# Performance work log

Measured on AMD Instinct MI355X. Metric: run time of the kernel, lower is better.

Reference implementation:

```python
import jax, jax.numpy as jnp
import numpy as np

N_HEAD = 16
N_KV_GROUP = 4
WINDOW = 256


def setup_inputs() -> dict:
    key = jax.random.key(0)
    ks = jax.random.split(key, 5)
    B, T, C = 2, 2048, 1024
    KV = C // N_HEAD * N_KV_GROUP  # 256
    s = 0.02
    return {
        "x": jax.random.normal(ks[0], (B, T, C), jnp.float32),
        "Wq": jax.random.normal(ks[1], (C, C), jnp.float32) * s,
        "bq": jnp.zeros((C,), jnp.float32),
        "Wk": jax.random.normal(ks[2], (C, KV), jnp.float32) * s,
        "bk": jnp.zeros((KV,), jnp.float32),
        "Wv": jax.random.normal(ks[3], (C, KV), jnp.float32) * s,
        "bv": jnp.zeros((KV,), jnp.float32),
        "Wo": jax.random.normal(ks[4], (C, C), jnp.float32) * s,
        "bo": jnp.zeros((C,), jnp.float32),
    }


def reference(x, Wq, bq, Wk, bk, Wv, bv, Wo, bo):
    B, T, C = x.shape
    hd = C // N_HEAD  # head dim = 64
    n_rep = N_HEAD // N_KV_GROUP

    q = x @ Wq + bq                      # [B,T,C]
    k = x @ Wk + bk                      # [B,T,KV]
    v = x @ Wv + bv

    q = q.reshape(B, T, N_HEAD, hd).transpose(0, 2, 1, 3)       # [B,H,T,d]
    k = k.reshape(B, T, N_KV_GROUP, hd).transpose(0, 2, 1, 3)   # [B,G,T,d]
    v = v.reshape(B, T, N_KV_GROUP, hd).transpose(0, 2, 1, 3)

    # GQA: repeat_interleave kv heads along head dim
    k_rep = jnp.repeat(k, n_rep, axis=1)                         # [B,H,T,d]
    v_rep = jnp.repeat(v, n_rep, axis=1)

    att = jnp.einsum("bhqd,bhkd->bhqk", q, k_rep) / jnp.sqrt(jnp.float32(hd))

    # causal + sliding window band mask: q position i attends to j in [i-WINDOW, i]
    i = jnp.arange(T)[:, None]
    j = jnp.arange(T)[None, :]
    band = (j <= i) & (j >= i - WINDOW)                           # [T,T]
    att = jnp.where(band[None, None], att, jnp.float32(-jnp.inf))

    att = jax.nn.softmax(att, axis=-1)
    y = jnp.einsum("bhqk,bhkd->bhqd", att, v_rep)                 # [B,H,T,d]
    y = y.transpose(0, 2, 1, 3).reshape(B, T, C)
    return y @ Wo + bo
```

## Files before the change

kernel.cpp:

```cpp
#include <hip/hip_runtime.h>
#include <hip/hip_bf16.h>

#define TT 2048
#define CC 1024
#define KVD 256
#define QKVD 1536

typedef __bf16 bf16x8 __attribute__((ext_vector_type(8)));
typedef float f32x4 __attribute__((ext_vector_type(4)));

__device__ __forceinline__ void gload_lds16(const __hip_bfloat16* g, __hip_bfloat16* l) {
  __builtin_amdgcn_global_load_lds(
      (const __attribute__((address_space(1))) unsigned int*)g,
      (__attribute__((address_space(3))) unsigned int*)l, 16, 0, 0);
}


__global__ __launch_bounds__(256) void k_prep(const float* __restrict__ x,
                                              const float* __restrict__ Wq,
                                              const float* __restrict__ Wk,
                                              const float* __restrict__ Wv,
                                              const float* __restrict__ Wo,
                                              const float* __restrict__ bq,
                                              const float* __restrict__ bk,
                                              const float* __restrict__ bv,
                                              __hip_bfloat16* __restrict__ xbf,
                                              __hip_bfloat16* __restrict__ wqkvT,
                                              __hip_bfloat16* __restrict__ woT,
                                              float* __restrict__ bqkv) {
  const int bxid = blockIdx.x;
  if (bxid < 4096) {
    size_t idx = ((size_t)bxid * 256 + threadIdx.x) * 4;
    float4 v = *(const float4*)(x + idx);
    xbf[idx + 0] = __float2bfloat16(v.x);
    xbf[idx + 1] = __float2bfloat16(v.y);
    xbf[idx + 2] = __float2bfloat16(v.z);
    xbf[idx + 3] = __float2bfloat16(v.w);
    return;
  }
  if (bxid == 4736) {
    for (int i = threadIdx.x; i < 1536; i += 256) {
      float v;
      if (i < 1024)      v = bq[i];
      else if (i < 1280) v = bk[i - 1024];
      else               v = bv[i - 1280];
      bqkv[i] = v;
    }
    return;
  }
  __shared__ float tile[64][65];
  const float* src;
  int ncols, k0, n0;
  __hip_bfloat16* dst;
  if (bxid < 4480) {
    const int idx = bxid - 4096;
    k0 = (idx & 15) * 64;
    n0 = (idx >> 4) * 64;
    dst = wqkvT;
    if (n0 < 1024)      { src = Wq; ncols = 1024; }
    else if (n0 < 1280) { src = Wk - 1024; ncols = 256; }
    else                { src = Wv - 1280; ncols = 256; }
  } else {
    const int idx = bxid - 4480;
    k0 = (idx & 15) * 64;
    n0 = (idx >> 4) * 64;
    dst = woT; src = Wo; ncols = 1024;
  }
  const int rw = threadIdx.x >> 6;
  const int cl = threadIdx.x & 63;
#pragma unroll
  for (int i = 0; i < 16; ++i) {
    const int kr = rw + i * 4;
    tile[kr][cl] = src[(size_t)(k0 + kr) * ncols + n0 + cl];
  }
  __syncthreads();
#pragma unroll
  for (int i = 0; i < 16; ++i) {
    const int nr = rw + i * 4;
    dst[(size_t)(n0 + nr) * 1024 + k0 + cl] = __float2bfloat16(tile[cl][nr]);
  }
}


__global__ __launch_bounds__(256, 3) void k_gemm1(const __hip_bfloat16* __restrict__ A,
                                                  const __hip_bfloat16* __restrict__ BT,
                                                  const float* __restrict__ bias,
                                                  __hip_bfloat16* __restrict__ C,
                                                  __hip_bfloat16* __restrict__ vtg) {
  __shared__ __hip_bfloat16 As[128][64];
  __shared__ __hip_bfloat16 Bs[128][64];

  const int tid  = threadIdx.x;
  const int m0   = blockIdx.y * 128;
  const int n0   = blockIdx.x * 128;
  const int w    = tid >> 6;
  const int lane = tid & 63;
  const int quad = lane >> 4;
  const int l16  = lane & 15;
  const int wm   = (w >> 1) * 64;
  const int wn   = (w & 1) * 64;

  const int dl_r = lane >> 3;
  const int dl_c = (lane & 7) ^ dl_r;

  const __hip_bfloat16* gA = A + (size_t)(m0 + w * 32 + dl_r) * 1024 + dl_c * 8;
  const __hip_bfloat16* gB = BT + (size_t)(n0 + w * 32 + dl_r) * 1024 + dl_c * 8;

  f32x4 acc[4][4] = {};

  for (int kt = 0; kt < 16; ++kt) {
    const int k0 = kt << 6;
#pragma unroll
    for (int rr = 0; rr < 4; ++rr) {
      gload_lds16(gA + k0 + (size_t)(rr * 8) * 1024, &As[w * 32 + rr * 8][0]);
      gload_lds16(gB + k0 + (size_t)(rr * 8) * 1024, &Bs[w * 32 + rr * 8][0]);
    }
    __syncthreads();

#pragma unroll
    for (int ks = 0; ks < 2; ++ks) {
      const int cb = (ks << 2) + quad;
      bf16x8 fa[4], fb[4];
#pragma unroll
      for (int i = 0; i < 4; ++i)
        fa[i] = *(const bf16x8*)&As[wm + i * 16 + l16][(cb ^ (l16 & 7)) << 3];
#pragma unroll
      for (int j = 0; j < 4; ++j)
        fb[j] = *(const bf16x8*)&Bs[wn + j * 16 + l16][(cb ^ (l16 & 7)) << 3];
#pragma unroll
      for (int i = 0; i < 4; ++i)
#pragma unroll
        for (int j = 0; j < 4; ++j)
          acc[i][j] = __builtin_amdgcn_mfma_f32_16x16x32_bf16(fa[i], fb[j], acc[i][j], 0, 0, 0);
    }
    __syncthreads();
  }

#pragma unroll
  for (int j = 0; j < 4; ++j) {
    const int gn = n0 + wn + j * 16 + l16;
    const float bias_v = bias[gn];
    if (gn >= 1280) {
      const int dfull = gn - 1280;
      const int gg = dfull >> 6;
      const int dd = dfull & 63;
#pragma unroll
      for (int i = 0; i < 4; ++i) {
        const int gm = m0 + wm + i * 16 + quad * 4;
        const int bb = gm >> 11;
        const int tl = gm & 2047;
        __hip_bfloat16 tmp[4];
#pragma unroll
        for (int r = 0; r < 4; ++r) tmp[r] = __float2bfloat16(acc[i][j][r] + bias_v);
        *(uint2*)(vtg + ((size_t)((bb * 4 + gg) * 64 + dd)) * TT + tl) = *(const uint2*)tmp;
      }
    } else {
#pragma unroll
      for (int i = 0; i < 4; ++i) {
        const int gmb = m0 + wm + i * 16 + quad * 4;
#pragma unroll
        for (int r = 0; r < 4; ++r)
          C[(size_t)(gmb + r) * QKVD + gn] = __float2bfloat16(acc[i][j][r] + bias_v);
      }
    }
  }
}


__global__ __launch_bounds__(256, 4) void k_gemm2(const __hip_bfloat16* __restrict__ A,
                                                  const __hip_bfloat16* __restrict__ BT,
                                                  const float* __restrict__ bias,
                                                  float* __restrict__ C) {
  __shared__ __hip_bfloat16 As[64][64];
  __shared__ __hip_bfloat16 Bs[128][64];

  const int tid  = threadIdx.x;
  const int m0   = blockIdx.y * 64;
  const int n0   = blockIdx.x * 128;
  const int w    = tid >> 6;
  const int lane = tid & 63;
  const int quad = lane >> 4;
  const int l16  = lane & 15;
  const int wm   = (w >> 1) * 32;
  const int wn   = (w & 1) * 64;

  const int dl_r = lane >> 3;
  const int dl_c = (lane & 7) ^ dl_r;

  const __hip_bfloat16* gA = A + (size_t)(m0 + w * 16 + dl_r) * 1024 + dl_c * 8;
  const __hip_bfloat16* gB = BT + (size_t)(n0 + w * 32 + dl_r) * 1024 + dl_c * 8;

  f32x4 acc[2][4] = {};

  for (int kt = 0; kt < 16; ++kt) {
    const int k0 = kt << 6;
    gload_lds16(gA + k0,                     &As[w * 16][0]);
    gload_lds16(gA + k0 + (size_t)8 * 1024,  &As[w * 16 + 8][0]);
    gload_lds16(gB + k0,                     &Bs[w * 32][0]);
    gload_lds16(gB + k0 + (size_t)8 * 1024,  &Bs[w * 32 + 8][0]);
    gload_lds16(gB + k0 + (size_t)16 * 1024, &Bs[w * 32 + 16][0]);
    gload_lds16(gB + k0 + (size_t)24 * 1024, &Bs[w * 32 + 24][0]);
    __syncthreads();

#pragma unroll
    for (int ks = 0; ks < 2; ++ks) {
      const int cb = (ks << 2) + quad;
      bf16x8 fa[2], fb[4];
#pragma unroll
      for (int i = 0; i < 2; ++i)
        fa[i] = *(const bf16x8*)&As[wm + i * 16 + l16][(cb ^ (l16 & 7)) << 3];
#pragma unroll
      for (int j = 0; j < 4; ++j)
        fb[j] = *(const bf16x8*)&Bs[wn + j * 16 + l16][(cb ^ (l16 & 7)) << 3];
#pragma unroll
      for (int i = 0; i < 2; ++i)
#pragma unroll
        for (int j = 0; j < 4; ++j)
          acc[i][j] = __builtin_amdgcn_mfma_f32_16x16x32_bf16(fa[i], fb[j], acc[i][j], 0, 0, 0);
    }
    __syncthreads();
  }

#pragma unroll
  for (int j = 0; j < 4; ++j) {
    const int gn = n0 + wn + j * 16 + l16;
    const float bias_v = bias[gn];
#pragma unroll
    for (int i = 0; i < 2; ++i) {
      const int gmb = m0 + wm + i * 16 + quad * 4;
#pragma unroll
      for (int r = 0; r < 4; ++r)
        C[(size_t)(gmb + r) * CC + gn] = acc[i][j][r] + bias_v;
    }
  }
}


__global__ __launch_bounds__(256) void k_attn(const __hip_bfloat16* __restrict__ qkv,
                                              const __hip_bfloat16* __restrict__ vtg,
                                              __hip_bfloat16* __restrict__ y) {
  __shared__ __hip_bfloat16 Kb[2][64][64];
  __shared__ __hip_bfloat16 Vb[2][64][64];
  __shared__ __hip_bfloat16 Ps[4][16][72];

  const int t    = threadIdx.x;
  const int w    = t >> 6;
  const int lane = t & 63;
  const int quad = lane >> 4;
  const int l16  = lane & 15;
  const int bx   = blockIdx.x;
  const int h    = blockIdx.y;
  const int b    = blockIdx.z;
  const int g    = h >> 2;
  const int i0   = bx * 64;
  const int qrow      = i0 + w * 16 + l16;
  const int my_q_base = i0 + w * 16 + quad * 4;

  const int lrow = lane >> 3;
  const int cgl  = (lane & 7) ^ lrow;

  const __hip_bfloat16* kg =
      qkv + ((size_t)(b * TT + w * 16 + lrow)) * QKVD + 1024 + g * 64 + cgl * 8;
  const __hip_bfloat16* vg =
      vtg + ((size_t)((b * 4 + g) * 64 + w * 16 + lrow)) * TT + cgl * 8;

  bf16x8 fq[2];
  {
    const __hip_bfloat16* qp = qkv + ((size_t)(b * TT + qrow)) * QKVD + h * 64 + quad * 8;
    fq[0] = *(const bf16x8*)qp;
    fq[1] = *(const bf16x8*)(qp + 32);
  }

  float l_r[4] = {0.f, 0.f, 0.f, 0.f};
  f32x4 o_acc[4] = {};
  const float EC = 0.125f * 1.44269504f;

  const int c_lo = bx >= 4 ? bx - 4 : 0;

  {
    const size_t ko = (size_t)(c_lo * 64) * QKVD;
    gload_lds16(kg + ko,                    &Kb[0][w * 16][0]);
    gload_lds16(kg + ko + (size_t)8 * QKVD, &Kb[0][w * 16 + 8][0]);
    const int vo = c_lo * 64;
    gload_lds16(vg + vo,                  &Vb[0][w * 16][0]);
    gload_lds16(vg + vo + (size_t)8 * TT, &Vb[0][w * 16 + 8][0]);
  }

  int buf = 0;
  for (int c = c_lo; c <= bx; ++c) {
    __syncthreads();
    if (c < bx) {
      const size_t ko = (size_t)((c + 1) * 64) * QKVD;
      gload_lds16(kg + ko,                    &Kb[buf ^ 1][w * 16][0]);
      gload_lds16(kg + ko + (size_t)8 * QKVD, &Kb[buf ^ 1][w * 16 + 8][0]);
      const int vo = (c + 1) * 64;
      gload_lds16(vg + vo,                  &Vb[buf ^ 1][w * 16][0]);
      gload_lds16(vg + vo + (size_t)8 * TT, &Vb[buf ^ 1][w * 16 + 8][0]);
    }

    const int jc = c * 64;

    f32x4 sacc[4] = {};
#pragma unroll
    for (int ks = 0; ks < 2; ++ks) {
      const int sw = (((ks << 2) + quad) ^ (l16 & 7)) << 3;
#pragma unroll
      for (int nt = 0; nt < 4; ++nt) {
        const bf16x8 fk = *(const bf16x8*)&Kb[buf][nt * 16 + l16][sw];
        sacc[nt] = __builtin_amdgcn_mfma_f32_16x16x32_bf16(fq[ks], fk, sacc[nt], 0, 0, 0);
      }
    }

    if (c == bx) {
#pragma unroll
      for (int r = 0; r < 4; ++r) {
        const int gi = my_q_base + r;
#pragma unroll
        for (int nt = 0; nt < 4; ++nt) {
          const int key = jc + nt * 16 + l16;
          const float p = (key <= gi) ? exp2f(sacc[nt][r] * EC) : 0.f;
          l_r[r] += p;
          Ps[w][quad * 4 + r][nt * 16 + l16] = __float2bfloat16(p);
        }
      }
    } else if (bx >= 4 && c == c_lo) {
#pragma unroll
      for (int r = 0; r < 4; ++r) {
        const int glo = my_q_base + r - 256;
#pragma unroll
        for (int nt = 0; nt < 4; ++nt) {
          const int key = jc + nt * 16 + l16;
          const float p = (key >= glo) ? exp2f(sacc[nt][r] * EC) : 0.f;
          l_r[r] += p;
          Ps[w][quad * 4 + r][nt * 16 + l16] = __float2bfloat16(p);
        }
      }
    } else {
#pragma unroll
      for (int r = 0; r < 4; ++r)
#pragma unroll
        for (int nt = 0; nt < 4; ++nt) {
          const float p = exp2f(sacc[nt][r] * EC);
          l_r[r] += p;
          Ps[w][quad * 4 + r][nt * 16 + l16] = __float2bfloat16(p);
        }
    }

    const bf16x8 fp0 = *(const bf16x8*)&Ps[w][l16][quad * 8];
    const bf16x8 fp1 = *(const bf16x8*)&Ps[w][l16][32 + quad * 8];

#pragma unroll
    for (int ks = 0; ks < 2; ++ks) {
      const int sw = (((ks << 2) + quad) ^ (l16 & 7)) << 3;
#pragma unroll
      for (int jt = 0; jt < 4; ++jt) {
        const bf16x8 fv = *(const bf16x8*)&Vb[buf][jt * 16 + l16][sw];
        o_acc[jt] = __builtin_amdgcn_mfma_f32_16x16x32_bf16(ks == 0 ? fp0 : fp1, fv,
                                                            o_acc[jt], 0, 0, 0);
      }
    }
    buf ^= 1;
  }

#pragma unroll
  for (int r = 0; r < 4; ++r) {
#pragma unroll
    for (int d = 1; d < 16; d <<= 1) l_r[r] += __shfl_xor(l_r[r], d);
    const float inv = 1.f / l_r[r];
    __hip_bfloat16* yp = y + ((size_t)(b * TT + my_q_base + r)) * CC + h * 64 + l16;
#pragma unroll
    for (int jt = 0; jt < 4; ++jt)
      yp[jt * 16] = __float2bfloat16(o_acc[jt][r] * inv);
  }
}


extern "C" void kernel_launch(void* const* d_in, const int* in_sizes, int n_in,
                              void* d_out, int out_size, void* d_ws, size_t ws_size,
                              hipStream_t stream) {
  const float* x  = (const float*)d_in[0];
  const float* Wq = (const float*)d_in[1];
  const float* bq = (const float*)d_in[2];
  const float* Wk = (const float*)d_in[3];
  const float* bk = (const float*)d_in[4];
  const float* Wv = (const float*)d_in[5];
  const float* bv = (const float*)d_in[6];
  const float* Wo = (const float*)d_in[7];
  const float* bo = (const float*)d_in[8];
  float* out = (float*)d_out;

  char* ws = (char*)d_ws;
  const size_t M = 2 * TT;
  __hip_bfloat16* xbf   = (__hip_bfloat16*)(ws);
  __hip_bfloat16* qkv   = (__hip_bfloat16*)(ws + 8388608);
  __hip_bfloat16* ybf   = (__hip_bfloat16*)(ws + 20971520);
  __hip_bfloat16* wqkvT = (__hip_bfloat16*)(ws + 29360128);
  __hip_bfloat16* woT   = (__hip_bfloat16*)(ws + 32505856);
  float*          bqkv  = (float*)(ws + 34603008);
  __hip_bfloat16* vtg   = (__hip_bfloat16*)(ws + 34609152);

  k_prep<<<4737, 256, 0, stream>>>(x, Wq, Wk, Wv, Wo, bq, bk, bv,
                                   xbf, wqkvT, woT, bqkv);

  k_gemm1<<<dim3(QKVD / 128, M / 128), 256, 0, stream>>>(xbf, wqkvT, bqkv, qkv, vtg);

  k_attn<<<dim3(TT / 64, 16, 2), 256, 0, stream>>>(qkv, vtg, ybf);

  k_gemm2<<<dim3(CC / 128, M / 64), 256, 0, stream>>>(ybf, woT, bo, out);
}
```

Measured before the change: 145.5 us.

## Give each attention wave two query tiles and halve the block size

```diff
diff --git a/kernel.cpp b/kernel.cpp
--- a/kernel.cpp
+++ b/kernel.cpp
@@ -236,12 +236,12 @@
 }
 
 
-__global__ __launch_bounds__(256) void k_attn(const __hip_bfloat16* __restrict__ qkv,
+__global__ __launch_bounds__(128) void k_attn(const __hip_bfloat16* __restrict__ qkv,
                                               const __hip_bfloat16* __restrict__ vtg,
                                               __hip_bfloat16* __restrict__ y) {
   __shared__ __hip_bfloat16 Kb[2][64][64];
   __shared__ __hip_bfloat16 Vb[2][64][64];
-  __shared__ __hip_bfloat16 Ps[4][16][72];
+  __shared__ __hip_bfloat16 Ps[2][32][72];
 
   const int t    = threadIdx.x;
   const int w    = t >> 6;
@@ -253,37 +253,38 @@
   const int b    = blockIdx.z;
   const int g    = h >> 2;
   const int i0   = bx * 64;
-  const int qrow      = i0 + w * 16 + l16;
-  const int my_q_base = i0 + w * 16 + quad * 4;
 
   const int lrow = lane >> 3;
   const int cgl  = (lane & 7) ^ lrow;
 
   const __hip_bfloat16* kg =
-      qkv + ((size_t)(b * TT + w * 16 + lrow)) * QKVD + 1024 + g * 64 + cgl * 8;
+      qkv + ((size_t)(b * TT + w * 32 + lrow)) * QKVD + 1024 + g * 64 + cgl * 8;
   const __hip_bfloat16* vg =
-      vtg + ((size_t)((b * 4 + g) * 64 + w * 16 + lrow)) * TT + cgl * 8;
-
-  bf16x8 fq[2];
-  {
+      vtg + ((size_t)((b * 4 + g) * 64 + w * 32 + lrow)) * TT + cgl * 8;
+
+  bf16x8 fq[2][2];
+#pragma unroll
+  for (int it = 0; it < 2; ++it) {
+    const int qrow = i0 + w * 32 + it * 16 + l16;
     const __hip_bfloat16* qp = qkv + ((size_t)(b * TT + qrow)) * QKVD + h * 64 + quad * 8;
-    fq[0] = *(const bf16x8*)qp;
-    fq[1] = *(const bf16x8*)(qp + 32);
-  }
-
-  float l_r[4] = {0.f, 0.f, 0.f, 0.f};
-  f32x4 o_acc[4] = {};
+    fq[it][0] = *(const bf16x8*)qp;
+    fq[it][1] = *(const bf16x8*)(qp + 32);
+  }
+
+  float l_r[2][4] = {};
+  f32x4 o_acc[2][4] = {};
   const float EC = 0.125f * 1.44269504f;
 
   const int c_lo = bx >= 4 ? bx - 4 : 0;
 
   {
     const size_t ko = (size_t)(c_lo * 64) * QKVD;
-    gload_lds16(kg + ko,                    &Kb[0][w * 16][0]);
-    gload_lds16(kg + ko + (size_t)8 * QKVD, &Kb[0][w * 16 + 8][0]);
     const int vo = c_lo * 64;
-    gload_lds16(vg + vo,                  &Vb[0][w * 16][0]);
-    gload_lds16(vg + vo + (size_t)8 * TT, &Vb[0][w * 16 + 8][0]);
+#pragma unroll
+    for (int rr = 0; rr < 4; ++rr) {
+      gload_lds16(kg + ko + (size_t)(rr * 8) * QKVD, &Kb[0][w * 32 + rr * 8][0]);
+      gload_lds16(vg + vo + (size_t)(rr * 8) * TT,   &Vb[0][w * 32 + rr * 8][0]);
+    }
   }
 
   int buf = 0;
@@ -291,86 +292,106 @@
     __syncthreads();
     if (c < bx) {
       const size_t ko = (size_t)((c + 1) * 64) * QKVD;
-      gload_lds16(kg + ko,                    &Kb[buf ^ 1][w * 16][0]);
-      gload_lds16(kg + ko + (size_t)8 * QKVD, &Kb[buf ^ 1][w * 16 + 8][0]);
       const int vo = (c + 1) * 64;
-      gload_lds16(vg + vo,                  &Vb[buf ^ 1][w * 16][0]);
-      gload_lds16(vg + vo + (size_t)8 * TT, &Vb[buf ^ 1][w * 16 + 8][0]);
+#pragma unroll
+      for (int rr = 0; rr < 4; ++rr) {
+        gload_lds16(kg + ko + (size_t)(rr * 8) * QKVD, &Kb[buf ^ 1][w * 32 + rr * 8][0]);
+        gload_lds16(vg + vo + (size_t)(rr * 8) * TT,   &Vb[buf ^ 1][w * 32 + rr * 8][0]);
+      }
     }
 
     const int jc = c * 64;
 
-    f32x4 sacc[4] = {};
+    f32x4 sacc[2][4] = {};
+    __builtin_amdgcn_s_setprio(1);
 #pragma unroll
     for (int ks = 0; ks < 2; ++ks) {
       const int sw = (((ks << 2) + quad) ^ (l16 & 7)) << 3;
 #pragma unroll
       for (int nt = 0; nt < 4; ++nt) {
         const bf16x8 fk = *(const bf16x8*)&Kb[buf][nt * 16 + l16][sw];
-        sacc[nt] = __builtin_amdgcn_mfma_f32_16x16x32_bf16(fq[ks], fk, sacc[nt], 0, 0, 0);
-      }
-    }
-
-    if (c == bx) {
-#pragma unroll
-      for (int r = 0; r < 4; ++r) {
-        const int gi = my_q_base + r;
-#pragma unroll
-        for (int nt = 0; nt < 4; ++nt) {
-          const int key = jc + nt * 16 + l16;
-          const float p = (key <= gi) ? exp2f(sacc[nt][r] * EC) : 0.f;
-          l_r[r] += p;
-          Ps[w][quad * 4 + r][nt * 16 + l16] = __float2bfloat16(p);
+#pragma unroll
+        for (int it = 0; it < 2; ++it)
+          sacc[it][nt] = __builtin_amdgcn_mfma_f32_16x16x32_bf16(fq[it][ks], fk, sacc[it][nt], 0, 0, 0);
+      }
+    }
+    __builtin_amdgcn_s_setprio(0);
+
+#pragma unroll
+    for (int it = 0; it < 2; ++it) {
+      const int my_q_base = i0 + w * 32 + it * 16 + quad * 4;
+      if (c == bx) {
+#pragma unroll
+        for (int r = 0; r < 4; ++r) {
+          const int gi = my_q_base + r;
+#pragma unroll
+          for (int nt = 0; nt < 4; ++nt) {
+            const int key = jc + nt * 16 + l16;
+            const float p = (key <= gi) ? exp2f(sacc[it][nt][r] * EC) : 0.f;
+            l_r[it][r] += p;
+            Ps[w][it * 16 + quad * 4 + r][nt * 16 + l16] = __float2bfloat16(p);
+          }
         }
-      }
-    } else if (bx >= 4 && c == c_lo) {
-#pragma unroll
-      for (int r = 0; r < 4; ++r) {
-        const int glo = my_q_base + r - 256;
-#pragma unroll
-        for (int nt = 0; nt < 4; ++nt) {
-          const int key = jc + nt * 16 + l16;
-          const float p = (key >= glo) ? exp2f(sacc[nt][r] * EC) : 0.f;
-          l_r[r] += p;
-          Ps[w][quad * 4 + r][nt * 16 + l16] = __float2bfloat16(p);
+      } else if (bx >= 4 && c == c_lo) {
+#pragma unroll
+        for (int r = 0; r < 4; ++r) {
+          const int glo = my_q_base + r - 256;
+#pragma unroll
+          for (int nt = 0; nt < 4; ++nt) {
+            const int key = jc + nt * 16 + l16;
+            const float p = (key >= glo) ? exp2f(sacc[it][nt][r] * EC) : 0.f;
+            l_r[it][r] += p;
+            Ps[w][it * 16 + quad * 4 + r][nt * 16 + l16] = __float2bfloat16(p);
+          }
         }
-      }
-    } else {
-#pragma unroll
-      for (int r = 0; r < 4; ++r)
-#pragma unroll
-        for (int nt = 0; nt < 4; ++nt) {
-          const float p = exp2f(sacc[nt][r] * EC);
-          l_r[r] += p;
-          Ps[w][quad * 4 + r][nt * 16 + l16] = __float2bfloat16(p);
-        }
-    }
-
-    const bf16x8 fp0 = *(const bf16x8*)&Ps[w][l16][quad * 8];
-    const bf16x8 fp1 = *(const bf16x8*)&Ps[w][l16][32 + quad * 8];
-
+      } else {
+#pragma unroll
+        for (int r = 0; r < 4; ++r)
+#pragma unroll
+          for (int nt = 0; nt < 4; ++nt) {
+            const float p = exp2f(sacc[it][nt][r] * EC);
+            l_r[it][r] += p;
+            Ps[w][it * 16 + quad * 4 + r][nt * 16 + l16] = __float2bfloat16(p);
+          }
+      }
+    }
+
+    bf16x8 fp[2][2];
+#pragma unroll
+    for (int it = 0; it < 2; ++it) {
+      fp[it][0] = *(const bf16x8*)&Ps[w][it * 16 + l16][quad * 8];
+      fp[it][1] = *(const bf16x8*)&Ps[w][it * 16 + l16][32 + quad * 8];
+    }
+
+    __builtin_amdgcn_s_setprio(1);
 #pragma unroll
     for (int ks = 0; ks < 2; ++ks) {
       const int sw = (((ks << 2) + quad) ^ (l16 & 7)) << 3;
 #pragma unroll
       for (int jt = 0; jt < 4; ++jt) {
         const bf16x8 fv = *(const bf16x8*)&Vb[buf][jt * 16 + l16][sw];
-        o_acc[jt] = __builtin_amdgcn_mfma_f32_16x16x32_bf16(ks == 0 ? fp0 : fp1, fv,
-                                                            o_acc[jt], 0, 0, 0);
-      }
-    }
+#pragma unroll
+        for (int it = 0; it < 2; ++it)
+          o_acc[it][jt] = __builtin_amdgcn_mfma_f32_16x16x32_bf16(fp[it][ks], fv, o_acc[it][jt], 0, 0, 0);
+      }
+    }
+    __builtin_amdgcn_s_setprio(0);
     buf ^= 1;
   }
 
 #pragma unroll
-  for (int r = 0; r < 4; ++r) {
-#pragma unroll
-    for (int d = 1; d < 16; d <<= 1) l_r[r] += __shfl_xor(l_r[r], d);
-    const float inv = 1.f / l_r[r];
-    __hip_bfloat16* yp = y + ((size_t)(b * TT + my_q_base + r)) * CC + h * 64 + l16;
-#pragma unroll
-    for (int jt = 0; jt < 4; ++jt)
-      yp[jt * 16] = __float2bfloat16(o_acc[jt][r] * inv);
+  for (int it = 0; it < 2; ++it) {
+#pragma unroll
+    for (int r = 0; r < 4; ++r) {
+#pragma unroll
+      for (int d = 1; d < 16; d <<= 1) l_r[it][r] += __shfl_xor(l_r[it][r], d);
+      const float inv = 1.f / l_r[it][r];
+      const int my_q_base = i0 + w * 32 + it * 16 + quad * 4;
+      __hip_bfloat16* yp = y + ((size_t)(b * TT + my_q_base + r)) * CC + h * 64 + l16;
+#pragma unroll
+      for (int jt = 0; jt < 4; ++jt)
+        yp[jt * 16] = __float2bfloat16(o_acc[it][jt][r] * inv);
+    }
   }
 }
 
@@ -404,7 +425,7 @@
 
   k_gemm1<<<dim3(QKVD / 128, M / 128), 256, 0, stream>>>(xbf, wqkvT, bqkv, qkv, vtg);
 
-  k_attn<<<dim3(TT / 64, 16, 2), 256, 0, stream>>>(qkv, vtg, ybf);
+  k_attn<<<dim3(TT / 64, 16, 2), 128, 0, stream>>>(qkv, vtg, ybf);
 
   k_gemm2<<<dim3(CC / 128, M / 64), 256, 0, stream>>>(ybf, woT, bo, out);
 }
```

Result: slower. 154.2 us (+6.0%).

## Load K/V fragments directly from global into registers, drop LDS double buffer

Applied to the files above, without the earlier changes.

```diff
diff --git a/kernel.cpp b/kernel.cpp
--- a/kernel.cpp
+++ b/kernel.cpp
@@ -239,8 +239,6 @@
 __global__ __launch_bounds__(256) void k_attn(const __hip_bfloat16* __restrict__ qkv,
                                               const __hip_bfloat16* __restrict__ vtg,
                                               __hip_bfloat16* __restrict__ y) {
-  __shared__ __hip_bfloat16 Kb[2][64][64];
-  __shared__ __hip_bfloat16 Vb[2][64][64];
   __shared__ __hip_bfloat16 Ps[4][16][72];
 
   const int t    = threadIdx.x;
@@ -256,13 +254,10 @@
   const int qrow      = i0 + w * 16 + l16;
   const int my_q_base = i0 + w * 16 + quad * 4;
 
-  const int lrow = lane >> 3;
-  const int cgl  = (lane & 7) ^ lrow;
-
   const __hip_bfloat16* kg =
-      qkv + ((size_t)(b * TT + w * 16 + lrow)) * QKVD + 1024 + g * 64 + cgl * 8;
+      qkv + ((size_t)(b * TT + l16)) * QKVD + 1024 + g * 64 + quad * 8;
   const __hip_bfloat16* vg =
-      vtg + ((size_t)((b * 4 + g) * 64 + w * 16 + lrow)) * TT + cgl * 8;
+      vtg + ((size_t)((b * 4 + g) * 64 + l16)) * TT + quad * 8;
 
   bf16x8 fq[2];
   {
@@ -277,39 +272,32 @@
 
   const int c_lo = bx >= 4 ? bx - 4 : 0;
 
-  {
-    const size_t ko = (size_t)(c_lo * 64) * QKVD;
-    gload_lds16(kg + ko,                    &Kb[0][w * 16][0]);
-    gload_lds16(kg + ko + (size_t)8 * QKVD, &Kb[0][w * 16 + 8][0]);
-    const int vo = c_lo * 64;
-    gload_lds16(vg + vo,                  &Vb[0][w * 16][0]);
-    gload_lds16(vg + vo + (size_t)8 * TT, &Vb[0][w * 16 + 8][0]);
-  }
-
-  int buf = 0;
   for (int c = c_lo; c <= bx; ++c) {
-    __syncthreads();
-    if (c < bx) {
-      const size_t ko = (size_t)((c + 1) * 64) * QKVD;
-      gload_lds16(kg + ko,                    &Kb[buf ^ 1][w * 16][0]);
-      gload_lds16(kg + ko + (size_t)8 * QKVD, &Kb[buf ^ 1][w * 16 + 8][0]);
-      const int vo = (c + 1) * 64;
-      gload_lds16(vg + vo,                  &Vb[buf ^ 1][w * 16][0]);
-      gload_lds16(vg + vo + (size_t)8 * TT, &Vb[buf ^ 1][w * 16 + 8][0]);
-    }
-
     const int jc = c * 64;
+    const __hip_bfloat16* kgc = kg + (size_t)jc * QKVD;
+    const __hip_bfloat16* vgc = vg + jc;
 
     f32x4 sacc[4] = {};
-#pragma unroll
-    for (int ks = 0; ks < 2; ++ks) {
-      const int sw = (((ks << 2) + quad) ^ (l16 & 7)) << 3;
-#pragma unroll
-      for (int nt = 0; nt < 4; ++nt) {
-        const bf16x8 fk = *(const bf16x8*)&Kb[buf][nt * 16 + l16][sw];
-        sacc[nt] = __builtin_amdgcn_mfma_f32_16x16x32_bf16(fq[ks], fk, sacc[nt], 0, 0, 0);
-      }
-    }
+    bf16x8 fk[2][4];
+#pragma unroll
+    for (int ks = 0; ks < 2; ++ks)
+#pragma unroll
+      for (int nt = 0; nt < 4; ++nt)
+        fk[ks][nt] = *(const bf16x8*)(kgc + (size_t)(nt * 16) * QKVD + ks * 32);
+    __builtin_amdgcn_s_setprio(1);
+#pragma unroll
+    for (int ks = 0; ks < 2; ++ks)
+#pragma unroll
+      for (int nt = 0; nt < 4; ++nt)
+        sacc[nt] = __builtin_amdgcn_mfma_f32_16x16x32_bf16(fq[ks], fk[ks][nt], sacc[nt], 0, 0, 0);
+    __builtin_amdgcn_s_setprio(0);
+
+    bf16x8 fv[2][4];
+#pragma unroll
+    for (int ks = 0; ks < 2; ++ks)
+#pragma unroll
+      for (int jt = 0; jt < 4; ++jt)
+        fv[ks][jt] = *(const bf16x8*)(vgc + (size_t)(jt * 16) * TT + ks * 32);
 
     if (c == bx) {
 #pragma unroll
@@ -349,17 +337,14 @@
     const bf16x8 fp0 = *(const bf16x8*)&Ps[w][l16][quad * 8];
     const bf16x8 fp1 = *(const bf16x8*)&Ps[w][l16][32 + quad * 8];
 
-#pragma unroll
-    for (int ks = 0; ks < 2; ++ks) {
-      const int sw = (((ks << 2) + quad) ^ (l16 & 7)) << 3;
-#pragma unroll
-      for (int jt = 0; jt < 4; ++jt) {
-        const bf16x8 fv = *(const bf16x8*)&Vb[buf][jt * 16 + l16][sw];
-        o_acc[jt] = __builtin_amdgcn_mfma_f32_16x16x32_bf16(ks == 0 ? fp0 : fp1, fv,
+    __builtin_amdgcn_s_setprio(1);
+#pragma unroll
+    for (int ks = 0; ks < 2; ++ks)
+#pragma unroll
+      for (int jt = 0; jt < 4; ++jt)
+        o_acc[jt] = __builtin_amdgcn_mfma_f32_16x16x32_bf16(ks == 0 ? fp0 : fp1, fv[ks][jt],
                                                             o_acc[jt], 0, 0, 0);
-      }
-    }
-    buf ^= 1;
+    __builtin_amdgcn_s_setprio(0);
   }
 
 #pragma unroll
```

After: 168.6 us. +15.9%, slower.
